# Optimization experiments

Measured on AMD Instinct MI355X. Metric: run time of the kernel, lower is better.

The kernel has to match this reference:

```python
import jax, jax.numpy as jnp
import numpy as np

# ---- fixed problem dimensions ----
B, S, T = 64, 200, 32          # batch of sequences, trees per seq, nodes per tree
V, E, C = 50000, 128, 128      # vocab, embedding_dim, encode_dim
H, OUT = 100, 104              # GRU hidden, output_dim
N = B * S * T                  # total nodes
D_MAX = 5                      # max depth of a 32-node complete binary tree


def setup_inputs() -> dict:
    key = jax.random.key(0)
    ks = jax.random.split(key, 16)
    # --- tree structure: every tree is a complete binary tree with T nodes ---
    local_parent = np.array([0] + [(i - 1) // 2 for i in range(1, T)], dtype=np.int64)
    local_depth = np.array([int(np.floor(np.log2(i + 1))) for i in range(T)], dtype=np.int64)
    num_trees = B * S
    offsets = np.arange(num_trees, dtype=np.int64) * T
    node_parent = (offsets[:, None] + local_parent[None, :]).reshape(-1)
    node_depth = np.tile(local_depth, num_trees)
    node_tree = np.repeat(np.arange(num_trees, dtype=np.int64), T)
    node_tokens = jax.random.randint(ks[0], (N,), 0, V, dtype=jnp.int64)
    sc = 0.05
    inp = {
        "node_tokens": node_tokens,
        "node_parent": jnp.asarray(node_parent),
        "node_tree": jnp.asarray(node_tree),
        "node_depth": jnp.asarray(node_depth),
        "emb": jax.random.normal(ks[1], (V, E), jnp.float32) * sc,
        "w_lin": jax.random.normal(ks[2], (C, E), jnp.float32) * sc,
        "b_lin": jnp.zeros((C,), jnp.float32),
        "w_ih_f": jax.random.normal(ks[3], (3 * H, C), jnp.float32) * sc,
        "w_hh_f": jax.random.normal(ks[4], (3 * H, H), jnp.float32) * sc,
        "b_ih_f": jnp.zeros((3 * H,), jnp.float32),
        "b_hh_f": jnp.zeros((3 * H,), jnp.float32),
        "w_ih_b": jax.random.normal(ks[5], (3 * H, C), jnp.float32) * sc,
        "w_hh_b": jax.random.normal(ks[6], (3 * H, H), jnp.float32) * sc,
        "b_ih_b": jnp.zeros((3 * H,), jnp.float32),
        "b_hh_b": jnp.zeros((3 * H,), jnp.float32),
        "fc_w": jax.random.normal(ks[7], (OUT, 2 * H), jnp.float32) * sc,
        "fc_b": jnp.zeros((OUT,), jnp.float32),
    }
    return inp


def _gru(x_sbc, w_ih, w_hh, b_ih, b_hh):
    """Torch-convention GRU over leading time axis. x_sbc: [S, B, C] -> [S, B, H]."""
    h0 = jnp.zeros((x_sbc.shape[1], w_hh.shape[1]), x_sbc.dtype)

    def step(h, xt):
        gx = xt @ w_ih.T + b_ih
        gh = h @ w_hh.T + b_hh
        xr, xz, xn = jnp.split(gx, 3, axis=-1)
        hr, hz, hn = jnp.split(gh, 3, axis=-1)
        r = jax.nn.sigmoid(xr + hr)
        z = jax.nn.sigmoid(xz + hz)
        n = jnp.tanh(xn + r * hn)
        h_new = (1.0 - z) * n + z * h
        return h_new, h_new

    _, hs = jax.lax.scan(step, h0, x_sbc)
    return hs


def reference(node_tokens, node_parent, node_tree, node_depth,
              emb, w_lin, b_lin,
              w_ih_f, w_hh_f, b_ih_f, b_hh_f,
              w_ih_b, w_hh_b, b_ih_b, b_hh_b,
              fc_w, fc_b):
    # per-node contribution: W * emb(token) + b   (recursion base of hidden_state)
    c = emb[node_tokens] @ w_lin.T + b_lin               # [N, C]
    # level-batched bottom-up scatter-add: h(node) = c(node) + sum(h(children))
    h = c
    for d in range(D_MAX, 0, -1):
        mask = (node_depth == d)[:, None]
        h = h.at[node_parent].add(jnp.where(mask, h, 0.0))
    # per-tree max pool over all node hidden states (TreeEncoder output)
    tree_vec = jax.ops.segment_max(h, node_tree, num_segments=B * S)  # [B*S, C]
    x = tree_vec.reshape(B, S, C)
    # bidirectional GRU (batch_first in torch; scan over time here)
    x_t = jnp.transpose(x, (1, 0, 2))                    # [S, B, C]
    fwd = _gru(x_t, w_ih_f, w_hh_f, b_ih_f, b_hh_f)      # [S, B, H]
    bwd = _gru(x_t[::-1], w_ih_b, w_hh_b, b_ih_b, b_hh_b)[::-1]
    gru_out = jnp.concatenate([fwd, bwd], axis=-1)       # [S, B, 2H]
    pool = gru_out.max(axis=0)                           # [B, 2H] (max over time)
    return pool @ fc_w.T + fc_b                          # [B, OUT]
```

## Files before the change

kernel.cpp:

```cpp
#include <hip/hip_runtime.h>
#include <hip/hip_bf16.h>
#include <math.h>

#define BB 64
#define SS 200
#define TT 32
#define EE 128
#define CC 128
#define HH 100
#define G3 300
#define OUTD 104
#define NTREE (BB*SS)

typedef __attribute__((ext_vector_type(4))) float f32x4;
typedef _Float16 f16x8 __attribute__((ext_vector_type(8)));

__device__ inline float fast_sigmoid(float x) {
    return __builtin_amdgcn_rcpf(1.f + __builtin_amdgcn_exp2f(-1.4426950408889634f * x));
}
__device__ inline float fast_tanh(float x) {
    return 1.f - 2.f * __builtin_amdgcn_rcpf(1.f + __builtin_amdgcn_exp2f(2.8853900817779268f * x));
}

#define BAR() asm volatile("s_waitcnt lgkmcnt(0)\n\ts_barrier" ::: "memory")


__global__ __launch_bounds__(256) void k0_prep(const float* __restrict__ w_lin,
                                               const float* __restrict__ w_ih_f,
                                               const float* __restrict__ w_ih_b,
                                               _Float16* __restrict__ wl,
                                               _Float16* __restrict__ k2b) {
    const int tid  = threadIdx.x;
    const int wave = tid >> 6;
    const int lane = tid & 63;
    const int r = lane & 15;
    const int q = lane >> 4;
    if (blockIdx.x == 0) {
#pragma unroll
        for (int nt = 0; nt < 2; ++nt)
#pragma unroll
            for (int kt = 0; kt < 4; ++kt) {
                const int n = wave * 32 + nt * 16 + r;
                const float* src = w_lin + (long)n * EE + kt * 32 + q * 8;
                f16x8 f;
#pragma unroll
                for (int e = 0; e < 8; ++e) f[e] = (_Float16)src[e];
                *(f16x8*)&wl[(size_t)((((wave * 2 + nt) * 4 + kt) * 64) + lane) * 8] = f;
            }
    } else {
        const int nb = blockIdx.x - 1;
        const int n = nb * 64 + wave * 16 + r;
        const int dir = (n >= 320) ? 1 : 0;
        const int j = n - dir * 320;
        const int jj = (j < G3) ? j : 0;
        const float* w = dir ? w_ih_b : w_ih_f;
#pragma unroll
        for (int kt = 0; kt < 4; ++kt) {
            const float* src = w + (long)jj * EE + kt * 32 + q * 8;
            f16x8 f;
#pragma unroll
            for (int e = 0; e < 8; ++e) f[e] = (_Float16)src[e];
            *(f16x8*)&k2b[(size_t)((((nb * 4 + wave) * 4 + kt) * 64) + lane) * 8] = f;
        }
    }
}

#define K1_TPI 2
#define AROWS (K1_TPI*TT)
#define LDA 136
#define LDC 132

__global__ __launch_bounds__(256) void k1_mfma(const int* __restrict__ tok,
                                               const float* __restrict__ emb,
                                               const _Float16* __restrict__ wl,
                                               const float* __restrict__ b_lin,
                                               _Float16* __restrict__ thi) {
    __shared__ __align__(16) _Float16 A_sh[AROWS * LDA];
    __shared__ __align__(16) float C_sh[AROWS * LDC];
    __shared__ int tok_sh[AROWS];

    const int tid  = threadIdx.x;
    const int wave = tid >> 6;
    const int lane = tid & 63;
    const int r = lane & 15;
    const int q = lane >> 4;

    f16x8 bfrag[2][4];
    float bias[2];
#pragma unroll
    for (int nt = 0; nt < 2; ++nt) {
        bias[nt] = b_lin[wave * 32 + nt * 16 + r];
#pragma unroll
        for (int kt = 0; kt < 4; ++kt)
            bfrag[nt][kt] = *(const f16x8*)&wl[(size_t)((((wave * 2 + nt) * 4 + kt) * 64) + lane) * 8];
    }

    const int tree0 = blockIdx.x * K1_TPI;
    if (tid < AROWS) tok_sh[tid] = tok[tree0 * TT + tid];
    __syncthreads();

#pragma unroll
    for (int i = 0; i < 8; ++i) {
        const int idx = tid + i * 256;
        const int row = idx >> 5;
        const int p   = idx & 31;
        const float4 e = ((const float4*)(emb + (long)tok_sh[row] * EE))[p];
        _Float16* dst = &A_sh[row * LDA + p * 4];
        dst[0] = (_Float16)e.x; dst[1] = (_Float16)e.y;
        dst[2] = (_Float16)e.z; dst[3] = (_Float16)e.w;
    }
    __syncthreads();

    f32x4 acc[4][2];
#pragma unroll
    for (int mt = 0; mt < 4; ++mt)
#pragma unroll
        for (int nt = 0; nt < 2; ++nt) acc[mt][nt] = (f32x4)(0.f);

#pragma unroll
    for (int mt = 0; mt < 4; ++mt) {
        const int m = mt * 16 + r;
        f16x8 afrag[4];
#pragma unroll
        for (int kt = 0; kt < 4; ++kt)
            afrag[kt] = *(const f16x8*)&A_sh[m * LDA + kt * 32 + q * 8];
#pragma unroll
        for (int nt = 0; nt < 2; ++nt)
#pragma unroll
            for (int kt = 0; kt < 4; ++kt)
                acc[mt][nt] = __builtin_amdgcn_mfma_f32_16x16x32_f16(
                    afrag[kt], bfrag[nt][kt], acc[mt][nt], 0, 0, 0);
    }

#pragma unroll
    for (int mt = 0; mt < 4; ++mt)
#pragma unroll
        for (int nt = 0; nt < 2; ++nt) {
            const int col = wave * 32 + nt * 16 + r;
#pragma unroll
            for (int reg = 0; reg < 4; ++reg) {
                const int row = mt * 16 + q * 4 + reg;
                C_sh[row * LDC + col] = acc[mt][nt][reg] + bias[nt];
            }
        }
    __syncthreads();

    {
        const int t = tid >> 7;
        const int j = tid & 127;
        const float* base = &C_sh[(t * TT) * LDC + j];
        float v[TT];
#pragma unroll
        for (int n = 0; n < TT; ++n) v[n] = base[n * LDC];
        float mx = -1e30f;
#pragma unroll
        for (int n = TT - 1; n >= 1; --n) {
            mx = fmaxf(mx, v[n]);
            v[(n - 1) >> 1] += v[n];
        }
        mx = fmaxf(mx, v[0]);
        thi[(size_t)(tree0 + t) * CC + j] = (_Float16)mx;
    }
}

__global__ __launch_bounds__(256) void k2_mfma(const _Float16* __restrict__ thi,
                                               const _Float16* __restrict__ k2b,
                                               const float* __restrict__ b_ih_f,
                                               const float* __restrict__ b_ih_b,
                                               float* __restrict__ gx) {
    __shared__ __align__(16) _Float16 Ah[32 * LDA];

    const int tid  = threadIdx.x;
    const int wave = tid >> 6;
    const int lane = tid & 63;
    const int r = lane & 15;
    const int q = lane >> 4;

    const int nb = blockIdx.x % 10;
    const int mb = blockIdx.x / 10;
    const int m0 = mb * 32;
    const int n0 = nb * 64;

#pragma unroll
    for (int i = 0; i < 2; ++i) {
        const int idx = tid + i * 256;
        const int row = idx >> 4;
        const int p   = idx & 15;
        f16x8 v = *(const f16x8*)&thi[(size_t)(m0 + row) * CC + p * 8];
        *(f16x8*)&Ah[row * LDA + p * 8] = v;
    }
    f16x8 bh[4];
#pragma unroll
    for (int kt = 0; kt < 4; ++kt)
        bh[kt] = *(const f16x8*)&k2b[(size_t)((((nb * 4 + wave) * 4 + kt) * 64) + lane) * 8];
    __syncthreads();

    f32x4 acc[2];
    acc[0] = (f32x4)(0.f); acc[1] = (f32x4)(0.f);
#pragma unroll
    for (int mt = 0; mt < 2; ++mt) {
        const int m = mt * 16 + r;
#pragma unroll
        for (int kt = 0; kt < 4; ++kt) {
            f16x8 a = *(const f16x8*)&Ah[m * LDA + kt * 32 + q * 8];
            acc[mt] = __builtin_amdgcn_mfma_f32_16x16x32_f16(a, bh[kt], acc[mt], 0, 0, 0);
        }
    }

    const int ng  = n0 + wave * 16 + r;
    const int dir = (ng >= 320) ? 1 : 0;
    const int j   = ng - dir * 320;
    const bool valid = (j < G3);
    const float bias = valid ? (dir ? b_ih_b[j] : b_ih_f[j]) : 0.f;
    float* gxd = gx + (long)dir * NTREE * G3;
    if (valid) {
#pragma unroll
        for (int mt = 0; mt < 2; ++mt)
#pragma unroll
            for (int reg = 0; reg < 4; ++reg) {
                const int m = m0 + mt * 16 + q * 4 + reg;
                gxd[(long)m * G3 + j] = acc[mt][reg] + bias;
            }
    }
}

__global__ __launch_bounds__(256, 1) void k3_gru(const float* __restrict__ gx,
                                                 const float* __restrict__ w_hh_f,
                                                 const float* __restrict__ b_hh_f,
                                                 const float* __restrict__ w_hh_b,
                                                 const float* __restrict__ b_hh_b,
                                                 float* __restrict__ pool) {
    const int bid = blockIdx.x;
    const int dir = bid & 1;
    const int b = bid >> 1;
    const float* w_hh = dir ? w_hh_b : w_hh_f;
    const float* b_hh = dir ? b_hh_b : b_hh_f;

    __shared__ __align__(16) _Float16 h_sh[2][128];
    __shared__ float g_sh[4][80];

    const int tid  = threadIdx.x;
    const int wave = tid >> 6;
    const int lane = tid & 63;
    const int r = lane & 15;
    const int q = lane >> 4;

    f16x8 bf[5][4];
#pragma unroll
    for (int i = 0; i < 5; ++i) {
        const int l = i * 16 + r;
        const int gate = l / 25;
        const int ch   = l - gate * 25;
        const bool nv  = (l < 75);
        const int row  = gate * HH + wave * 25 + ch;
#pragma unroll
        for (int kt = 0; kt < 4; ++kt) {
            f16x8 f;
#pragma unroll
            for (int e = 0; e < 8; ++e) {
                const int k = kt * 32 + q * 8 + e;
                f[e] = (_Float16)((nv && k < HH) ? w_hh[row * HH + k] : 0.f);
            }
            bf[i][kt] = f;
        }
    }

    const int m = lane;
    const int c = wave * 25 + m;
    const bool act = (m < 25);
    float br = 0.f, bz = 0.f, bn = 0.f;
    if (act) { br = b_hh[c]; bz = b_hh[HH + c]; bn = b_hh[2 * HH + c]; }

    if (tid < 128) { h_sh[0][tid] = (_Float16)0.f; h_sh[1][tid] = (_Float16)0.f; }

    const float* gxd = gx + (long)dir * NTREE * G3;
    const int sstep = dir ? -1 : 1;
    int s = dir ? (SS - 1) : 0;
    float xr = 0.f, xz = 0.f, xn = 0.f;
    if (act) {
        const float* row0 = gxd + ((long)b * SS + s) * G3;
        xr = row0[c]; xz = row0[HH + c]; xn = row0[2 * HH + c];
    }
    float hj = 0.f, hmax = -1e30f;
    __syncthreads();

    for (int t = 0; t < SS; ++t) {
        const int p = t & 1;
        const int s_n = s + sstep;
        float xrn = 0.f, xzn = 0.f, xnn = 0.f;
        if (act && t < SS - 1) {
            const float* row0 = gxd + ((long)b * SS + s_n) * G3;
            xrn = row0[c]; xzn = row0[HH + c]; xnn = row0[2 * HH + c];
        }

        f16x8 a[4];
#pragma unroll
        for (int kt = 0; kt < 4; ++kt)
            a[kt] = *(const f16x8*)&h_sh[p][kt * 32 + q * 8];
        f32x4 acc[5];
#pragma unroll
        for (int i = 0; i < 5; ++i) {
            acc[i] = (f32x4)(0.f);
#pragma unroll
            for (int kt = 0; kt < 4; ++kt)
                acc[i] = __builtin_amdgcn_mfma_f32_16x16x32_f16(a[kt], bf[i][kt], acc[i], 0, 0, 0);
        }
        if (q == 0) {
#pragma unroll
            for (int i = 0; i < 5; ++i)
                g_sh[wave][i * 16 + r] = acc[i][0];
        }
        if (act) {
            const float ghr = g_sh[wave][m];
            const float ghz = g_sh[wave][25 + m];
            const float ghn = g_sh[wave][50 + m];
            const float rg = fast_sigmoid(xr + ghr + br);
            const float zg = fast_sigmoid(xz + ghz + bz);
            const float ng = fast_tanh(xn + rg * (ghn + bn));
            hj = (1.f - zg) * ng + zg * hj;
            hmax = fmaxf(hmax, hj);
            h_sh[1 - p][c] = (_Float16)hj;
            xr = xrn; xz = xzn; xn = xnn;
        }
        BAR();
        s = s_n;
    }
    if (act) pool[(long)b * (2 * HH) + dir * HH + c] = hmax;
}

__global__ __launch_bounds__(256) void k4_fc(const float* __restrict__ pool,
                                             const float* __restrict__ fc_w,
                                             const float* __restrict__ fc_b,
                                             float* __restrict__ out) {
    const int b = blockIdx.x;
    __shared__ __align__(16) float p_sh[2 * HH];
    const int t = threadIdx.x;
    if (t < 2 * HH) p_sh[t] = pool[(long)b * (2 * HH) + t];
    __syncthreads();
    if (t < OUTD) {
        const float4* wr4 = (const float4*)(fc_w + (long)t * (2 * HH));
        const float4* p4 = (const float4*)p_sh;
        float a0 = 0.f, a1 = 0.f;
#pragma unroll
        for (int k = 0; k < 50; k += 2) {
            float4 w0 = wr4[k],   p0 = p4[k];
            float4 w1 = wr4[k+1], p1 = p4[k+1];
            a0 += w0.x*p0.x + w0.y*p0.y + w0.z*p0.z + w0.w*p0.w;
            a1 += w1.x*p1.x + w1.y*p1.y + w1.z*p1.z + w1.w*p1.w;
        }
        out[(long)b * OUTD + t] = fc_b[t] + a0 + a1;
    }
}

extern "C" void kernel_launch(void* const* d_in, const int* in_sizes, int n_in,
                              void* d_out, int out_size, void* d_ws, size_t ws_size,
                              hipStream_t stream) {
    const int*   tok    = (const int*)d_in[0];
    const float* emb    = (const float*)d_in[4];
    const float* w_lin  = (const float*)d_in[5];
    const float* b_lin  = (const float*)d_in[6];
    const float* w_ih_f = (const float*)d_in[7];
    const float* w_hh_f = (const float*)d_in[8];
    const float* b_ih_f = (const float*)d_in[9];
    const float* b_hh_f = (const float*)d_in[10];
    const float* w_ih_b = (const float*)d_in[11];
    const float* w_hh_b = (const float*)d_in[12];
    const float* b_ih_b = (const float*)d_in[13];
    const float* b_hh_b = (const float*)d_in[14];
    const float* fc_w   = (const float*)d_in[15];
    const float* fc_b   = (const float*)d_in[16];

    char* wsb = (char*)d_ws;
    _Float16* wl   = (_Float16*)(wsb);
    _Float16* k2b  = (_Float16*)(wsb + 32768);
    _Float16* thi  = (_Float16*)(wsb + 196608);
    float*    gx   = (float*)(wsb + 3473408);
    float*    pool = (float*)(wsb);
    float*    out  = (float*)d_out;

    k0_prep<<<11, 256, 0, stream>>>(w_lin, w_ih_f, w_ih_b, wl, k2b);
    k1_mfma<<<NTREE / K1_TPI, 256, 0, stream>>>(tok, emb, wl, b_lin, thi);
    k2_mfma<<<(NTREE / 32) * 10, 256, 0, stream>>>(thi, k2b, b_ih_f, b_ih_b, gx);
    k3_gru <<<2 * BB, 256, 0, stream>>>(gx, w_hh_f, b_hh_f, w_hh_b, b_hh_b, pool);
    k4_fc  <<<BB, 256, 0, stream>>>(pool, fc_w, fc_b, out);
}
```

Measured before the change: 245.7 us.

## Compute tree subtree sums via MFMA with ancestor matrix instead of LDS reduction

```diff
diff --git a/kernel.cpp b/kernel.cpp
--- a/kernel.cpp
+++ b/kernel.cpp
@@ -20,6 +20,16 @@
 }
 __device__ inline float fast_tanh(float x) {
     return 1.f - 2.f * __builtin_amdgcn_rcpf(1.f + __builtin_amdgcn_exp2f(2.8853900817779268f * x));
+}
+__device__ inline unsigned pack2f16(float a, float b) {
+    union { _Float16 h[2]; unsigned u; } x;
+    x.h[0] = (_Float16)a; x.h[1] = (_Float16)b;
+    return x.u;
+}
+__device__ inline float subtree_cnt(int p) {
+    return (p == 0) ? 32.f : (p == 1) ? 16.f : (p == 2) ? 15.f :
+           (p == 3) ? 8.f  : (p <= 6) ? 7.f  : (p == 7) ? 4.f  :
+           (p <= 14) ? 3.f : (p == 15) ? 2.f : 1.f;
 }
 
 #define BAR() asm volatile("s_waitcnt lgkmcnt(0)\n\ts_barrier" ::: "memory")
@@ -65,19 +75,14 @@
     }
 }
 
-#define K1_TPI 2
-#define AROWS (K1_TPI*TT)
 #define LDA 136
-#define LDC 132
-
-__global__ __launch_bounds__(256) void k1_mfma(const int* __restrict__ tok,
-                                               const float* __restrict__ emb,
-                                               const _Float16* __restrict__ wl,
-                                               const float* __restrict__ b_lin,
-                                               _Float16* __restrict__ thi) {
-    __shared__ __align__(16) _Float16 A_sh[AROWS * LDA];
-    __shared__ __align__(16) float C_sh[AROWS * LDC];
-    __shared__ int tok_sh[AROWS];
+__global__ __launch_bounds__(512, 4) void k1_mfma(const int* __restrict__ tok,
+                                                  const float* __restrict__ emb,
+                                                  const _Float16* __restrict__ wl,
+                                                  const float* __restrict__ b_lin,
+                                                  _Float16* __restrict__ thi) {
+    __shared__ __align__(16) _Float16 A_sh[64 * LDA];
+    __shared__ int tok_sh[64];
 
     const int tid  = threadIdx.x;
     const int wave = tid >> 6;
@@ -85,81 +90,89 @@
     const int r = lane & 15;
     const int q = lane >> 4;
 
-    f16x8 bfrag[2][4];
-    float bias[2];
-#pragma unroll
-    for (int nt = 0; nt < 2; ++nt) {
-        bias[nt] = b_lin[wave * 32 + nt * 16 + r];
-#pragma unroll
-        for (int kt = 0; kt < 4; ++kt)
-            bfrag[nt][kt] = *(const f16x8*)&wl[(size_t)((((wave * 2 + nt) * 4 + kt) * 64) + lane) * 8];
-    }
-
-    const int tree0 = blockIdx.x * K1_TPI;
-    if (tid < AROWS) tok_sh[tid] = tok[tree0 * TT + tid];
-    __syncthreads();
-
-#pragma unroll
-    for (int i = 0; i < 8; ++i) {
-        const int idx = tid + i * 256;
-        const int row = idx >> 5;
-        const int p   = idx & 31;
-        const float4 e = ((const float4*)(emb + (long)tok_sh[row] * EE))[p];
-        _Float16* dst = &A_sh[row * LDA + p * 4];
-        dst[0] = (_Float16)e.x; dst[1] = (_Float16)e.y;
-        dst[2] = (_Float16)e.z; dst[3] = (_Float16)e.w;
-    }
-    __syncthreads();
-
-    f32x4 acc[4][2];
-#pragma unroll
-    for (int mt = 0; mt < 4; ++mt)
-#pragma unroll
-        for (int nt = 0; nt < 2; ++nt) acc[mt][nt] = (f32x4)(0.f);
-
+    f16x8 bfrag[4];
+#pragma unroll
+    for (int kt = 0; kt < 4; ++kt)
+        bfrag[kt] = *(const f16x8*)&wl[(size_t)(((wave * 4 + kt) * 64) + lane) * 8];
+    const float bias = b_lin[wave * 16 + r];
+
+    f16x8 l2f[2];
+#pragma unroll
+    for (int mt2 = 0; mt2 < 2; ++mt2) {
+        const int p = mt2 * 16 + r;
+#pragma unroll
+        for (int e = 0; e < 8; ++e) {
+            int x = q * 8 + e;
+            while (x > p) x = (x - 1) >> 1;
+            l2f[mt2][e] = (_Float16)((x == p) ? 1.f : 0.f);
+        }
+    }
+
+    const int tree0 = blockIdx.x * 2;
+    if (tid < 64) tok_sh[tid] = tok[tree0 * TT + tid];
+    __syncthreads();
+
+#pragma unroll
+    for (int i = 0; i < 2; ++i) {
+        const int idx = tid + i * 512;
+        const int row = idx >> 4;
+        const int p4  = idx & 15;
+        const float4* src = (const float4*)(emb + (long)tok_sh[row] * EE + p4 * 8);
+        const float4 e0 = src[0], e1 = src[1];
+        f16x8 v;
+        v[0] = (_Float16)e0.x; v[1] = (_Float16)e0.y; v[2] = (_Float16)e0.z; v[3] = (_Float16)e0.w;
+        v[4] = (_Float16)e1.x; v[5] = (_Float16)e1.y; v[6] = (_Float16)e1.z; v[7] = (_Float16)e1.w;
+        *(f16x8*)&A_sh[row * LDA + p4 * 8] = v;
+    }
+    __syncthreads();
+
+    unsigned pk[4][2];
 #pragma unroll
     for (int mt = 0; mt < 4; ++mt) {
         const int m = mt * 16 + r;
-        f16x8 afrag[4];
-#pragma unroll
-        for (int kt = 0; kt < 4; ++kt)
-            afrag[kt] = *(const f16x8*)&A_sh[m * LDA + kt * 32 + q * 8];
-#pragma unroll
-        for (int nt = 0; nt < 2; ++nt)
-#pragma unroll
-            for (int kt = 0; kt < 4; ++kt)
-                acc[mt][nt] = __builtin_amdgcn_mfma_f32_16x16x32_f16(
-                    afrag[kt], bfrag[nt][kt], acc[mt][nt], 0, 0, 0);
-    }
-
-#pragma unroll
-    for (int mt = 0; mt < 4; ++mt)
-#pragma unroll
-        for (int nt = 0; nt < 2; ++nt) {
-            const int col = wave * 32 + nt * 16 + r;
+        f32x4 acc = (f32x4)(0.f);
+#pragma unroll
+        for (int kt = 0; kt < 4; ++kt) {
+            f16x8 af = *(const f16x8*)&A_sh[m * LDA + kt * 32 + q * 8];
+            acc = __builtin_amdgcn_mfma_f32_16x16x32_f16(af, bfrag[kt], acc, 0, 0, 0);
+        }
+        pk[mt][0] = pack2f16(acc[0], acc[1]);
+        pk[mt][1] = pack2f16(acc[2], acc[3]);
+    }
+
+#pragma unroll
+    for (int t = 0; t < 2; ++t) {
+        const int l0 = (r + 16 * ((2 * q) & 3)) << 2;
+        const int l1 = (r + 16 * ((2 * q + 1) & 3)) << 2;
+        const bool hi = (q >> 1) != 0;
+        const unsigned x0 = __builtin_amdgcn_ds_bpermute(l0, (int)pk[2 * t][0]);
+        const unsigned y0 = __builtin_amdgcn_ds_bpermute(l0, (int)pk[2 * t + 1][0]);
+        const unsigned x1 = __builtin_amdgcn_ds_bpermute(l0, (int)pk[2 * t][1]);
+        const unsigned y1 = __builtin_amdgcn_ds_bpermute(l0, (int)pk[2 * t + 1][1]);
+        const unsigned x2 = __builtin_amdgcn_ds_bpermute(l1, (int)pk[2 * t][0]);
+        const unsigned y2 = __builtin_amdgcn_ds_bpermute(l1, (int)pk[2 * t + 1][0]);
+        const unsigned x3 = __builtin_amdgcn_ds_bpermute(l1, (int)pk[2 * t][1]);
+        const unsigned y3 = __builtin_amdgcn_ds_bpermute(l1, (int)pk[2 * t + 1][1]);
+        union { unsigned u[4]; f16x8 v; } b2;
+        b2.u[0] = hi ? y0 : x0;
+        b2.u[1] = hi ? y1 : x1;
+        b2.u[2] = hi ? y2 : x2;
+        b2.u[3] = hi ? y3 : x3;
+
+        float mx = -1e30f;
+#pragma unroll
+        for (int mt2 = 0; mt2 < 2; ++mt2) {
+            f32x4 a2 = __builtin_amdgcn_mfma_f32_16x16x32_f16(l2f[mt2], b2.v, (f32x4)(0.f), 0, 0, 0);
 #pragma unroll
             for (int reg = 0; reg < 4; ++reg) {
-                const int row = mt * 16 + q * 4 + reg;
-                C_sh[row * LDC + col] = acc[mt][nt][reg] + bias[nt];
+                const int p = mt2 * 16 + q * 4 + reg;
+                mx = fmaxf(mx, a2[reg] + subtree_cnt(p) * bias);
             }
         }
-    __syncthreads();
-
-    {
-        const int t = tid >> 7;
-        const int j = tid & 127;
-        const float* base = &C_sh[(t * TT) * LDC + j];
-        float v[TT];
-#pragma unroll
-        for (int n = 0; n < TT; ++n) v[n] = base[n * LDC];
-        float mx = -1e30f;
-#pragma unroll
-        for (int n = TT - 1; n >= 1; --n) {
-            mx = fmaxf(mx, v[n]);
-            v[(n - 1) >> 1] += v[n];
-        }
-        mx = fmaxf(mx, v[0]);
-        thi[(size_t)(tree0 + t) * CC + j] = (_Float16)mx;
+        mx = fmaxf(mx, __shfl_xor(mx, 16, 64));
+        mx = fmaxf(mx, __shfl_xor(mx, 32, 64));
+        if (q == 0)
+            thi[(size_t)(tree0 + t) * CC + wave * 16 + r] = (_Float16)mx;
     }
 }
 
@@ -379,7 +392,7 @@
     float*    out  = (float*)d_out;
 
     k0_prep<<<11, 256, 0, stream>>>(w_lin, w_ih_f, w_ih_b, wl, k2b);
-    k1_mfma<<<NTREE / K1_TPI, 256, 0, stream>>>(tok, emb, wl, b_lin, thi);
+    k1_mfma<<<NTREE / 2, 512, 0, stream>>>(tok, emb, wl, b_lin, thi);
     k2_mfma<<<(NTREE / 32) * 10, 256, 0, stream>>>(thi, k2b, b_ih_f, b_ih_b, gx);
     k3_gru <<<2 * BB, 256, 0, stream>>>(gx, w_hh_f, b_hh_f, w_hh_b, b_hh_b, pool);
     k4_fc  <<<BB, 256, 0, stream>>>(pool, fc_w, fc_b, out);
```

Result: slower. 257.8 us (+5.0%).
